# Kernel tuning notes

Hardware: AMD Instinct MI355X
Metric: run time of the kernel (lower is better)

The kernel has to match this reference:

```python
import jax, jax.numpy as jnp
import numpy as np

P = 196608  # number of sample points (N rays x D samples)
N = 2048    # number of rays
K = 8       # number of slot instances
ZD = 64     # network latent dim
N_FREQ = 5
N_FREQ_VIEW = 3
IN_DIM = 33 + 64   # pos-emb (33) + slot feat (64)
VIEW_DIM = 21      # view pos-emb


def sin_emb(x, n_freq):
    # x: (P, 3) -> (P, 3 + 3*2*n_freq); order per freq: sin then cos (matches torch loop)
    freqs = 2.0 ** jnp.arange(n_freq, dtype=x.dtype)          # linspace(0, n_freq-1, n_freq)
    xf = x[:, None, :] * freqs[None, :, None]                  # (P, F, 3)
    e = jnp.stack([jnp.sin(xf), jnp.cos(xf)], axis=2)          # (P, F, 2, 3)
    return jnp.concatenate([x, e.reshape(x.shape[0], -1)], axis=1)


def _lin(x, W, b):
    return x @ W.T + b


def setup_inputs() -> dict:
    key = jax.random.key(0)
    ks = iter(jax.random.split(key, 40))
    def W(o, i):
        return jax.random.normal(next(ks), (o, i), jnp.float32) * (1.0 / np.sqrt(i))
    def b(o):
        return jnp.zeros((o,), jnp.float32)
    inp = {
        "sampling_coor": jax.random.uniform(next(ks), (P, 3), jnp.float32, -1.0, 1.0),
        "sampling_view": jax.random.normal(next(ks), (N, 3), jnp.float32),
        "slots": jax.random.normal(next(ks), (1, K, 64), jnp.float32),
        "raw_density": jax.random.normal(next(ks), (K, P), jnp.float32),
        "act_shift": jnp.zeros((1,), jnp.float32),
        "Wb0": W(ZD, IN_DIM), "bb0": b(ZD),
        "Wb1": W(ZD, ZD), "bb1": b(ZD),
        "Wb2": W(ZD, ZD), "bb2": b(ZD),
        "Wa0": W(ZD, ZD + IN_DIM), "ba0": b(ZD),
        "Wa1": W(ZD, ZD), "ba1": b(ZD),
        "Wa2": W(ZD, ZD), "ba2": b(ZD),
        "Wl": W(ZD, ZD), "bl": b(ZD),                 # after_latent
        "Wv": W(ZD // 2, VIEW_DIM + ZD), "bv": b(ZD // 2),  # views_linears
        "Wc0": W(ZD // 4, ZD // 2), "bc0": b(ZD // 4),      # color[0]
        "Wc1": W(3, ZD // 4), "bc1": b(3),                  # color[2]
        "ray_id": jnp.sort(jax.random.randint(next(ks), (P,), 0, N)).astype(jnp.int64),
    }
    return inp


def reference(sampling_coor, sampling_view, slots, raw_density, act_shift,
              Wb0, bb0, Wb1, bb1, Wb2, bb2,
              Wa0, ba0, Wa1, ba1, Wa2, ba2,
              Wl, bl, Wv, bv, Wc0, bc0, Wc1, bc1,
              ray_id):
    Kk = raw_density.shape[0]
    Pp = sampling_coor.shape[0]
    relu = jax.nn.relu

    coor_emb = sin_emb(sampling_coor, N_FREQ)                    # (P, 33)
    view_emb = sin_emb(sampling_view, N_FREQ_VIEW)[ray_id, :]    # (P, 21) gathered per point

    # broadcast to (K, P, .) instead of flattening to (K*P, .)
    query_ex = jnp.broadcast_to(coor_emb[None], (Kk, Pp, coor_emb.shape[1]))
    slots_ex = jnp.broadcast_to(slots[0][:, None, :], (Kk, Pp, slots.shape[2]))
    inp = jnp.concatenate([query_ex, slots_ex], axis=-1)         # (K, P, 97)

    tmp = relu(_lin(inp, Wb0, bb0))
    tmp = relu(_lin(tmp, Wb1, bb1))
    tmp = relu(_lin(tmp, Wb2, bb2))
    tmp = relu(_lin(jnp.concatenate([inp, tmp], axis=-1), Wa0, ba0))  # skip concat (K,P,161)
    tmp = relu(_lin(tmp, Wa1, ba1))
    tmp = relu(_lin(tmp, Wa2, ba2))
    latent = _lin(tmp, Wl, bl)                                   # (K, P, 64)

    qv = jnp.broadcast_to(view_emb[None], (Kk, Pp, view_emb.shape[1]))
    h = relu(_lin(jnp.concatenate([latent, qv], axis=-1), Wv, bv))
    h = relu(_lin(h, Wc0, bc0))
    raw_rgb_logits = _lin(h, Wc1, bc1)                           # (K, P, 3)

    raw_masks = jax.nn.softplus(raw_density[..., None] + act_shift)  # (K, P, 1)
    raw_sigma = raw_masks                                        # dens_noise = 0.0
    raw_rgb = (jnp.tanh(raw_rgb_logits) + 1.0) / 2.0             # (K, P, 3)

    masks = raw_masks / (raw_masks.sum(axis=0) + 1e-5)           # (K, P, 1)
    raw_rgb_all = (raw_rgb * masks).sum(axis=0)                  # (P, 3)
    raw_sigma_all = (raw_sigma * masks).sum(axis=0)[..., 0]      # (P,)
    return (raw_rgb_all, raw_sigma_all, raw_rgb, raw_sigma[..., 0])
```

## Files before the change

### kernel.cpp

```cpp
#include <hip/hip_runtime.h>
#include <hip/hip_bf16.h>
#include <math.h>

#define PP 196608
#define NK 8

#define O_SIGALL 589824
#define O_RGB    786432
#define O_SIG    5505024

typedef __attribute__((ext_vector_type(8))) short short8;
typedef __attribute__((ext_vector_type(4))) float f32x4;
typedef __attribute__((ext_vector_type(4))) unsigned uint4v;

#define FBB0   0
#define FBA0   512
#define FBB1   1024
#define FBB2   1088
#define FBA1   1152
#define FBA2   1216
#define FBL    1280
#define FBV    1344
#define FBC0   1376
#define FBC1   1392
#define FW32B0 1408
#define FW32A0 1472

#define FB0 0
#define FB1 2048
#define FB2 6144
#define FA0 10240
#define FA1 16384
#define FA2 20480
#define FL  24576
#define FV  28672
#define FC0 31744
#define FC1 32256

#define WS_BYTES 71680

__device__ __forceinline__ short bfr(float f) {
    unsigned u = __builtin_bit_cast(unsigned, f);
    unsigned r = (u + 0x7FFFu + ((u >> 16) & 1u)) >> 16;
    return (short)r;
}

__device__ __forceinline__ unsigned pk2(float a, float b) {
    __hip_bfloat162 h = __float22bfloat162_rn(float2{a, b});
    unsigned r;
    __builtin_memcpy(&r, &h, sizeof(r));
    return r;
}

__device__ __forceinline__ int tau(int p) {
    return 16 * ((p >> 2) & 1) + 4 * (p >> 3) + (p & 3);
}

__device__ __forceinline__ float pe_elem(int j, float c0, float c1, float c2, int jmax) {
    int r = j - 3;
    int rf = r < 0 ? 0 : r;
    int f = rf / 6;
    int t = rf - 6 * f;
    int comp = (j < 3) ? j : (t >= 3 ? t - 3 : t);
    float c = (comp == 0) ? c0 : ((comp == 1) ? c1 : c2);
    float x = c * (float)(1 << f);
    float val = (t < 3) ? sinf(x) : cosf(x);
    if (j < 3) val = c;
    return (j < jmax) ? val : 0.f;
}

__device__ __forceinline__ float softplus_(float d) {
    return fmaxf(d, 0.f) + log1pf(expf(-fabsf(d)));
}

#define MFMA(a, b, c) __builtin_amdgcn_mfma_f32_16x16x32_bf16(a, b, c, 0, 0, 0)

__global__ void prep_kernel(
    const float* __restrict__ slots,
    const float* __restrict__ Wb0, const float* __restrict__ bb0,
    const float* __restrict__ Wb1, const float* __restrict__ bb1,
    const float* __restrict__ Wb2, const float* __restrict__ bb2,
    const float* __restrict__ Wa0, const float* __restrict__ ba0,
    const float* __restrict__ Wa1, const float* __restrict__ ba1,
    const float* __restrict__ Wa2, const float* __restrict__ ba2,
    const float* __restrict__ Wl,  const float* __restrict__ bl,
    const float* __restrict__ Wv,  const float* __restrict__ bv,
    const float* __restrict__ Wc0, const float* __restrict__ bc0,
    const float* __restrict__ Wc1, const float* __restrict__ bc1,
    char* __restrict__ ws)
{
    float* wsF = (float*)ws;
    short* wsS = (short*)(ws + 6144);
    const int tid = threadIdx.x;

    for (int idx = tid; idx < 512; idx += 256) {
        int k = idx >> 6, j = idx & 63;
        const float* sl = slots + k * 64;
        float a = bb0[j];
        const float* w0 = Wb0 + j * 97 + 33;
        for (int i = 0; i < 64; ++i) a = fmaf(w0[i], sl[i], a);
        wsF[FBB0 + idx] = a;
        float b = ba0[j];
        const float* w1 = Wa0 + j * 161 + 33;
        for (int i = 0; i < 64; ++i) b = fmaf(w1[i], sl[i], b);
        wsF[FBA0 + idx] = b;
    }
    for (int idx = tid; idx < 64; idx += 256) {
        wsF[FBB1 + idx] = bb1[idx];
        wsF[FBB2 + idx] = bb2[idx];
        wsF[FBA1 + idx] = ba1[idx];
        wsF[FBA2 + idx] = ba2[idx];
        wsF[FBL  + idx] = bl[idx];
        wsF[FW32B0 + idx] = Wb0[idx * 97 + 32];
        wsF[FW32A0 + idx] = Wa0[idx * 161 + 32];
        if (idx < 32) wsF[FBV + idx] = bv[idx];
        if (idx < 16) { wsF[FBC0 + idx] = bc0[idx];
                        wsF[FBC1 + idx] = (idx < 3) ? bc1[idx] : 0.f; }
    }
    for (int idx = tid; idx < 2048; idx += 256) {
        int frag = idx >> 9, rem = idx & 511, L = rem >> 3, i = rem & 7;
        int r = 16 * frag + (L & 15);
        int cif = 8 * (L >> 4) + i;
        wsS[FB0 + idx] = bfr(Wb0[r * 97 + tau(cif)]);
    }
#define PREP64(FOFF, W) \
    for (int idx = tid; idx < 4096; idx += 256) { \
        int frag = idx >> 9, rem = idx & 511, L = rem >> 3, i = rem & 7; \
        int t = frag >> 1, s = frag & 1; \
        int r = 16 * t + (L & 15); \
        int cif = 8 * (L >> 4) + i; \
        int C = 32 * s + cif; \
        int lc = (C & ~31) + tau(C & 31); \
        wsS[(FOFF) + idx] = bfr(W[r * 64 + lc]); }
    PREP64(FB1, Wb1)
    PREP64(FB2, Wb2)
    PREP64(FA1, Wa1)
    PREP64(FA2, Wa2)
    PREP64(FL,  Wl)
#undef PREP64
    for (int idx = tid; idx < 6144; idx += 256) {
        int frag = idx >> 9, rem = idx & 511, L = rem >> 3, i = rem & 7;
        int t = frag / 3, s = frag % 3;
        int r = 16 * t + (L & 15);
        int cif = 8 * (L >> 4) + i;
        float v;
        if (s == 0) v = Wa0[r * 161 + tau(cif)];
        else {
            int lc = (s == 1 ? 64 : 96) + tau(cif);
            v = Wa0[r * 161 + 33 + lc];
        }
        wsS[FA0 + idx] = bfr(v);
    }
    for (int idx = tid; idx < 3072; idx += 256) {
        int frag = idx >> 9, rem = idx & 511, L = rem >> 3, i = rem & 7;
        int t = frag / 3, s = frag % 3;
        int r = 16 * t + (L & 15);
        int cif = 8 * (L >> 4) + i;
        int C = 32 * s + cif;
        int lc = (C & ~31) + tau(C & 31);
        wsS[FV + idx] = bfr(lc < 85 ? Wv[r * 85 + lc] : 0.f);
    }
    for (int idx = tid; idx < 512; idx += 256) {
        int L = idx >> 3, i = idx & 7;
        int r = L & 15;
        int cif = 8 * (L >> 4) + i;
        int lc = tau(cif);
        wsS[FC0 + idx] = bfr(Wc0[r * 32 + lc]);
        wsS[FC1 + idx] = bfr((r < 3 && lc < 16) ? Wc1[r * 16 + lc] : 0.f);
    }
}

#define FRAG(base, f) (*(const short8*)(shS + (base) + (f) * 512 + l * 8))
#define BIA(off, t)   (*(const f32x4*)(shF + (off) + 16 * (t) + g4))

#define PACKP(cA, cB, dst) { uint4v u_; \
  u_[0] = pk2(fmaxf((cA)[0],0.f), fmaxf((cA)[1],0.f)); \
  u_[1] = pk2(fmaxf((cA)[2],0.f), fmaxf((cA)[3],0.f)); \
  u_[2] = pk2(fmaxf((cB)[0],0.f), fmaxf((cB)[1],0.f)); \
  u_[3] = pk2(fmaxf((cB)[2],0.f), fmaxf((cB)[3],0.f)); \
  dst = __builtin_bit_cast(short8, u_); }

#define PACKN(cA, cB, dst) { uint4v u_; \
  u_[0] = pk2((cA)[0], (cA)[1]); \
  u_[1] = pk2((cA)[2], (cA)[3]); \
  u_[2] = pk2((cB)[0], (cB)[1]); \
  u_[3] = pk2((cB)[2], (cB)[3]); \
  dst = __builtin_bit_cast(short8, u_); }

#define ADD32(c, wv) { (c)[0]=fmaf((wv)[0],cosv,(c)[0]); (c)[1]=fmaf((wv)[1],cosv,(c)[1]); \
                       (c)[2]=fmaf((wv)[2],cosv,(c)[2]); (c)[3]=fmaf((wv)[3],cosv,(c)[3]); }

#define LAYER64_1(FB, BOFF, PK) { \
  short8 A00=FRAG(FB,0), A01=FRAG(FB,1), A10=FRAG(FB,2), A11=FRAG(FB,3); \
  short8 A20=FRAG(FB,4), A21=FRAG(FB,5), A30=FRAG(FB,6), A31=FRAG(FB,7); \
  f32x4 c0=BIA(BOFF,0), c1=BIA(BOFF,1), c2=BIA(BOFF,2), c3=BIA(BOFF,3); \
  c0=MFMA(A00,p0,c0); c1=MFMA(A10,p0,c1); c2=MFMA(A20,p0,c2); c3=MFMA(A30,p0,c3); \
  c0=MFMA(A01,p1,c0); c1=MFMA(A11,p1,c1); c2=MFMA(A21,p1,c2); c3=MFMA(A31,p1,c3); \
  PK(c0,c1,p0); PK(c2,c3,p1); }

__global__ __launch_bounds__(512, 4) void decoder_kernel(
    const float* __restrict__ coor,
    const float* __restrict__ view,
    const float* __restrict__ dens,
    const float* __restrict__ act_shift,
    const int*   __restrict__ ray_id,
    const char*  __restrict__ ws,
    float* __restrict__ out)
{
    __shared__ __align__(16) char sh[WS_BYTES];
    const float* shF = (const float*)sh;
    const short* shS = (const short*)(sh + 6144);

    const int tid = threadIdx.x;
    const int l   = tid & 63;
    const int l15 = l & 15;
    const int g   = (l >> 4) & 3;
    const int g4  = g * 4;
    const int p   = blockIdx.x * 128 + (tid >> 6) * 16 + l15;

    {
        f32x4* dst = (f32x4*)sh;
        const f32x4* src = (const f32x4*)ws;
        for (int i = tid; i < WS_BYTES / 16; i += 512) dst[i] = src[i];
    }

    short8 embB0;
    float cosv;
    {
        float c0 = coor[p * 3 + 0], c1 = coor[p * 3 + 1], c2 = coor[p * 3 + 2];
        #pragma unroll
        for (int i = 0; i < 8; ++i) {
            int j = ((i >> 2) * 16) + 4 * g + (i & 3);
            embB0[i] = bfr(pe_elem(j, c0, c1, c2, 33));
        }
        cosv = cosf(c2 * 16.f);
    }
    short8 vembB;
    {
        int rid = ray_id[p];
        float v0 = view[rid * 3 + 0], v1 = view[rid * 3 + 1], v2 = view[rid * 3 + 2];
        #pragma unroll
        for (int i = 0; i < 8; ++i) {
            int j = ((i >> 2) * 16) + 4 * g + (i & 3);
            vembB[i] = bfr(pe_elem(j, v0, v1, v2, 21));
        }
    }
    float shift = act_shift[0];

    __syncthreads();

    #pragma unroll 1
    for (int k = 0; k < NK; ++k) {
        asm volatile("" ::: "memory");

        {
            float d_ = dens[k * PP + p] + shift;
            float sp = softplus_(d_);
            if (l < 16) out[O_SIG + k * PP + p] = sp;
        }

        short8 p0, p1;

        {
            short8 A0 = FRAG(FB0, 0), A1 = FRAG(FB0, 1), A2 = FRAG(FB0, 2), A3 = FRAG(FB0, 3);
            f32x4 wv0 = BIA(FW32B0, 0), wv1 = BIA(FW32B0, 1), wv2 = BIA(FW32B0, 2), wv3 = BIA(FW32B0, 3);
            f32x4 c0 = *(const f32x4*)(shF + FBB0 + k * 64 +  0 + g4);
            f32x4 c1 = *(const f32x4*)(shF + FBB0 + k * 64 + 16 + g4);
            f32x4 c2 = *(const f32x4*)(shF + FBB0 + k * 64 + 32 + g4);
            f32x4 c3 = *(const f32x4*)(shF + FBB0 + k * 64 + 48 + g4);
            c0 = MFMA(A0, embB0, c0); c1 = MFMA(A1, embB0, c1);
            c2 = MFMA(A2, embB0, c2); c3 = MFMA(A3, embB0, c3);
            ADD32(c0, wv0) ADD32(c1, wv1) ADD32(c2, wv2) ADD32(c3, wv3)
            PACKP(c0, c1, p0); PACKP(c2, c3, p1);
        }
        LAYER64_1(FB1, FBB1, PACKP)
        LAYER64_1(FB2, FBB2, PACKP)
        {
            short8 E0 = FRAG(FA0, 0), K00 = FRAG(FA0, 1),  K01 = FRAG(FA0, 2);
            short8 E1 = FRAG(FA0, 3), K10 = FRAG(FA0, 4),  K11 = FRAG(FA0, 5);
            short8 E2 = FRAG(FA0, 6), K20 = FRAG(FA0, 7),  K21 = FRAG(FA0, 8);
            short8 E3 = FRAG(FA0, 9), K30 = FRAG(FA0, 10), K31 = FRAG(FA0, 11);
            f32x4 wv0 = BIA(FW32A0, 0), wv1 = BIA(FW32A0, 1), wv2 = BIA(FW32A0, 2), wv3 = BIA(FW32A0, 3);
            f32x4 c0 = *(const f32x4*)(shF + FBA0 + k * 64 +  0 + g4);
            f32x4 c1 = *(const f32x4*)(shF + FBA0 + k * 64 + 16 + g4);
            f32x4 c2 = *(const f32x4*)(shF + FBA0 + k * 64 + 32 + g4);
            f32x4 c3 = *(const f32x4*)(shF + FBA0 + k * 64 + 48 + g4);
            c0 = MFMA(E0, embB0, c0); c1 = MFMA(E1, embB0, c1);
            c2 = MFMA(E2, embB0, c2); c3 = MFMA(E3, embB0, c3);
            c0 = MFMA(K00, p0, c0); c1 = MFMA(K10, p0, c1);
            c2 = MFMA(K20, p0, c2); c3 = MFMA(K30, p0, c3);
            c0 = MFMA(K01, p1, c0); c1 = MFMA(K11, p1, c1);
            c2 = MFMA(K21, p1, c2); c3 = MFMA(K31, p1, c3);
            ADD32(c0, wv0) ADD32(c1, wv1) ADD32(c2, wv2) ADD32(c3, wv3)
            PACKP(c0, c1, p0); PACKP(c2, c3, p1);
        }
        LAYER64_1(FA1, FBA1, PACKP)
        LAYER64_1(FA2, FBA2, PACKP)
        LAYER64_1(FL,  FBL,  PACKN)
        {
            f32x4 cv0 = BIA(FBV, 0), cv1 = BIA(FBV, 1);
            cv0 = MFMA(FRAG(FV, 0), p0, cv0);  cv1 = MFMA(FRAG(FV, 3), p0, cv1);
            cv0 = MFMA(FRAG(FV, 1), p1, cv0);  cv1 = MFMA(FRAG(FV, 4), p1, cv1);
            cv0 = MFMA(FRAG(FV, 2), vembB, cv0); cv1 = MFMA(FRAG(FV, 5), vembB, cv1);
            short8 vB;
            PACKP(cv0, cv1, vB);
            f32x4 cc = BIA(FBC0, 0);
            cc = MFMA(FRAG(FC0, 0), vB, cc);
            short8 cB;
            { uint4v u_;
              u_[0] = pk2(fmaxf(cc[0],0.f), fmaxf(cc[1],0.f));
              u_[1] = pk2(fmaxf(cc[2],0.f), fmaxf(cc[3],0.f));
              u_[2] = 0u; u_[3] = 0u;
              cB = __builtin_bit_cast(short8, u_); }
            f32x4 cf = BIA(FBC1, 0);
            cf = MFMA(FRAG(FC1, 0), cB, cf);
            if (l < 16) {
                int base = O_RGB + (k * PP + p) * 3;
                out[base + 0] = (tanhf(cf[0]) + 1.f) * 0.5f;
                out[base + 1] = (tanhf(cf[1]) + 1.f) * 0.5f;
                out[base + 2] = (tanhf(cf[2]) + 1.f) * 0.5f;
            }
        }
    }
}

__global__ __launch_bounds__(256) void reduce_kernel(float* __restrict__ out)
{
    const int p = blockIdx.x * 256 + threadIdx.x;
    float s0 = out[O_SIG + 0 * PP + p];
    float s1 = out[O_SIG + 1 * PP + p];
    float s2 = out[O_SIG + 2 * PP + p];
    float s3 = out[O_SIG + 3 * PP + p];
    float s4 = out[O_SIG + 4 * PP + p];
    float s5 = out[O_SIG + 5 * PP + p];
    float s6 = out[O_SIG + 6 * PP + p];
    float s7 = out[O_SIG + 7 * PP + p];
    float msum = s0 + s1 + s2 + s3 + s4 + s5 + s6 + s7;
    float inv = 1.f / (msum + 1e-5f);
    float mk2 = s0*s0 + s1*s1 + s2*s2 + s3*s3 + s4*s4 + s5*s5 + s6*s6 + s7*s7;
    out[O_SIGALL + p] = mk2 * inv;
    float a0 = 0.f, a1 = 0.f, a2 = 0.f;
#define RK(i, sv) { float wk = (sv) * inv; \
    int b_ = O_RGB + ((i) * PP + p) * 3; \
    a0 = fmaf(wk, out[b_ + 0], a0); \
    a1 = fmaf(wk, out[b_ + 1], a1); \
    a2 = fmaf(wk, out[b_ + 2], a2); }
    RK(0, s0) RK(1, s1) RK(2, s2) RK(3, s3)
    RK(4, s4) RK(5, s5) RK(6, s6) RK(7, s7)
#undef RK
    out[p * 3 + 0] = a0;
    out[p * 3 + 1] = a1;
    out[p * 3 + 2] = a2;
}

extern "C" void kernel_launch(void* const* d_in, const int* in_sizes, int n_in,
                              void* d_out, int out_size, void* d_ws, size_t ws_size,
                              hipStream_t stream) {
    const float* coor  = (const float*)d_in[0];
    const float* view  = (const float*)d_in[1];
    const float* slots = (const float*)d_in[2];
    const float* dens  = (const float*)d_in[3];
    const float* shf   = (const float*)d_in[4];
    const float* Wb0 = (const float*)d_in[5];  const float* bb0 = (const float*)d_in[6];
    const float* Wb1 = (const float*)d_in[7];  const float* bb1 = (const float*)d_in[8];
    const float* Wb2 = (const float*)d_in[9];  const float* bb2 = (const float*)d_in[10];
    const float* Wa0 = (const float*)d_in[11]; const float* ba0 = (const float*)d_in[12];
    const float* Wa1 = (const float*)d_in[13]; const float* ba1 = (const float*)d_in[14];
    const float* Wa2 = (const float*)d_in[15]; const float* ba2 = (const float*)d_in[16];
    const float* Wl  = (const float*)d_in[17]; const float* bl  = (const float*)d_in[18];
    const float* Wv  = (const float*)d_in[19]; const float* bv  = (const float*)d_in[20];
    const float* Wc0 = (const float*)d_in[21]; const float* bc0 = (const float*)d_in[22];
    const float* Wc1 = (const float*)d_in[23]; const float* bc1 = (const float*)d_in[24];
    const int*   ray = (const int*)d_in[25];
    float* out = (float*)d_out;

    prep_kernel<<<dim3(1), dim3(256), 0, stream>>>(
        slots, Wb0, bb0, Wb1, bb1, Wb2, bb2,
        Wa0, ba0, Wa1, ba1, Wa2, ba2,
        Wl, bl, Wv, bv, Wc0, bc0, Wc1, bc1, (char*)d_ws);

    decoder_kernel<<<dim3(PP / 128), dim3(512), 0, stream>>>(
        coor, view, dens, shf, ray, (const char*)d_ws, out);

    reduce_kernel<<<dim3(PP / 256), dim3(256), 0, stream>>>(out);
}
```

Measured before the change: 201.6 us.

## Process two slots per loop iteration to share weight fragment loads

```diff
diff --git a/kernel.cpp b/kernel.cpp
--- a/kernel.cpp
+++ b/kernel.cpp
@@ -172,6 +172,7 @@
 
 #define FRAG(base, f) (*(const short8*)(shS + (base) + (f) * 512 + l * 8))
 #define BIA(off, t)   (*(const f32x4*)(shF + (off) + 16 * (t) + g4))
+#define BSLOT(off, kidx, t) (*(const f32x4*)(shF + (off) + (kidx) * 64 + 16 * (t) + g4))
 
 #define PACKP(cA, cB, dst) { uint4v u_; \
   u_[0] = pk2(fmaxf((cA)[0],0.f), fmaxf((cA)[1],0.f)); \
@@ -190,13 +191,40 @@
 #define ADD32(c, wv) { (c)[0]=fmaf((wv)[0],cosv,(c)[0]); (c)[1]=fmaf((wv)[1],cosv,(c)[1]); \
                        (c)[2]=fmaf((wv)[2],cosv,(c)[2]); (c)[3]=fmaf((wv)[3],cosv,(c)[3]); }
 
-#define LAYER64_1(FB, BOFF, PK) { \
+#define LAYER64_2(FB, BOFF, PK) { \
   short8 A00=FRAG(FB,0), A01=FRAG(FB,1), A10=FRAG(FB,2), A11=FRAG(FB,3); \
   short8 A20=FRAG(FB,4), A21=FRAG(FB,5), A30=FRAG(FB,6), A31=FRAG(FB,7); \
-  f32x4 c0=BIA(BOFF,0), c1=BIA(BOFF,1), c2=BIA(BOFF,2), c3=BIA(BOFF,3); \
-  c0=MFMA(A00,p0,c0); c1=MFMA(A10,p0,c1); c2=MFMA(A20,p0,c2); c3=MFMA(A30,p0,c3); \
-  c0=MFMA(A01,p1,c0); c1=MFMA(A11,p1,c1); c2=MFMA(A21,p1,c2); c3=MFMA(A31,p1,c3); \
-  PK(c0,c1,p0); PK(c2,c3,p1); }
+  f32x4 b0_=BIA(BOFF,0), b1_=BIA(BOFF,1), b2_=BIA(BOFF,2), b3_=BIA(BOFF,3); \
+  f32x4 c0=b0_, c1=b1_, c2=b2_, c3=b3_; \
+  c0=MFMA(A00,p0a,c0); c1=MFMA(A10,p0a,c1); c2=MFMA(A20,p0a,c2); c3=MFMA(A30,p0a,c3); \
+  c0=MFMA(A01,p1a,c0); c1=MFMA(A11,p1a,c1); c2=MFMA(A21,p1a,c2); c3=MFMA(A31,p1a,c3); \
+  PK(c0,c1,p0a); PK(c2,c3,p1a); \
+  f32x4 d0=b0_, d1=b1_, d2=b2_, d3=b3_; \
+  d0=MFMA(A00,p0b,d0); d1=MFMA(A10,p0b,d1); d2=MFMA(A20,p0b,d2); d3=MFMA(A30,p0b,d3); \
+  d0=MFMA(A01,p1b,d0); d1=MFMA(A11,p1b,d1); d2=MFMA(A21,p1b,d2); d3=MFMA(A31,p1b,d3); \
+  PK(d0,d1,p0b); PK(d2,d3,p1b); }
+
+#define TAIL1(PA, PB, KIDX) { \
+  f32x4 cv0 = BIA(FBV, 0), cv1 = BIA(FBV, 1); \
+  cv0 = MFMA(AV00, PA, cv0); cv1 = MFMA(AV10, PA, cv1); \
+  cv0 = MFMA(AV01, PB, cv0); cv1 = MFMA(AV11, PB, cv1); \
+  cv0 = MFMA(AV02, vembB, cv0); cv1 = MFMA(AV12, vembB, cv1); \
+  short8 vB; PACKP(cv0, cv1, vB); \
+  f32x4 cc = BIA(FBC0, 0); \
+  cc = MFMA(AC0f, vB, cc); \
+  short8 cB; \
+  { uint4v u_; \
+    u_[0] = pk2(fmaxf(cc[0],0.f), fmaxf(cc[1],0.f)); \
+    u_[1] = pk2(fmaxf(cc[2],0.f), fmaxf(cc[3],0.f)); \
+    u_[2] = 0u; u_[3] = 0u; \
+    cB = __builtin_bit_cast(short8, u_); } \
+  f32x4 cf = BIA(FBC1, 0); \
+  cf = MFMA(AC1f, cB, cf); \
+  if (l < 16) { \
+      int base_ = O_RGB + ((KIDX) * PP + p) * 3; \
+      out[base_ + 0] = (tanhf(cf[0]) + 1.f) * 0.5f; \
+      out[base_ + 1] = (tanhf(cf[1]) + 1.f) * 0.5f; \
+      out[base_ + 2] = (tanhf(cf[2]) + 1.f) * 0.5f; } }
 
 __global__ __launch_bounds__(512, 4) void decoder_kernel(
     const float* __restrict__ coor,
@@ -250,76 +278,73 @@
     __syncthreads();
 
     #pragma unroll 1
-    for (int k = 0; k < NK; ++k) {
+    for (int kk = 0; kk < 4; ++kk) {
         asm volatile("" ::: "memory");
 
+        const int k0 = 2 * kk, k1 = 2 * kk + 1;
+
         {
-            float d_ = dens[k * PP + p] + shift;
-            float sp = softplus_(d_);
-            if (l < 16) out[O_SIG + k * PP + p] = sp;
-        }
-
-        short8 p0, p1;
+            float da = dens[k0 * PP + p] + shift;
+            float sa = softplus_(da);
+            if (l < 16) out[O_SIG + k0 * PP + p] = sa;
+            float db = dens[k1 * PP + p] + shift;
+            float sb = softplus_(db);
+            if (l < 16) out[O_SIG + k1 * PP + p] = sb;
+        }
+
+        short8 p0a, p1a, p0b, p1b;
 
         {
             short8 A0 = FRAG(FB0, 0), A1 = FRAG(FB0, 1), A2 = FRAG(FB0, 2), A3 = FRAG(FB0, 3);
             f32x4 wv0 = BIA(FW32B0, 0), wv1 = BIA(FW32B0, 1), wv2 = BIA(FW32B0, 2), wv3 = BIA(FW32B0, 3);
-            f32x4 c0 = *(const f32x4*)(shF + FBB0 + k * 64 +  0 + g4);
-            f32x4 c1 = *(const f32x4*)(shF + FBB0 + k * 64 + 16 + g4);
-            f32x4 c2 = *(const f32x4*)(shF + FBB0 + k * 64 + 32 + g4);
-            f32x4 c3 = *(const f32x4*)(shF + FBB0 + k * 64 + 48 + g4);
-            c0 = MFMA(A0, embB0, c0); c1 = MFMA(A1, embB0, c1);
-            c2 = MFMA(A2, embB0, c2); c3 = MFMA(A3, embB0, c3);
-            ADD32(c0, wv0) ADD32(c1, wv1) ADD32(c2, wv2) ADD32(c3, wv3)
-            PACKP(c0, c1, p0); PACKP(c2, c3, p1);
-        }
-        LAYER64_1(FB1, FBB1, PACKP)
-        LAYER64_1(FB2, FBB2, PACKP)
+            f32x4 z = {0.f, 0.f, 0.f, 0.f};
+            f32x4 t0 = MFMA(A0, embB0, z), t1 = MFMA(A1, embB0, z);
+            f32x4 t2 = MFMA(A2, embB0, z), t3 = MFMA(A3, embB0, z);
+            ADD32(t0, wv0) ADD32(t1, wv1) ADD32(t2, wv2) ADD32(t3, wv3)
+            f32x4 c0 = t0 + BSLOT(FBB0, k0, 0), c1 = t1 + BSLOT(FBB0, k0, 1);
+            f32x4 c2 = t2 + BSLOT(FBB0, k0, 2), c3 = t3 + BSLOT(FBB0, k0, 3);
+            PACKP(c0, c1, p0a); PACKP(c2, c3, p1a);
+            f32x4 d0 = t0 + BSLOT(FBB0, k1, 0), d1 = t1 + BSLOT(FBB0, k1, 1);
+            f32x4 d2 = t2 + BSLOT(FBB0, k1, 2), d3 = t3 + BSLOT(FBB0, k1, 3);
+            PACKP(d0, d1, p0b); PACKP(d2, d3, p1b);
+        }
+        LAYER64_2(FB1, FBB1, PACKP)
+        LAYER64_2(FB2, FBB2, PACKP)
         {
             short8 E0 = FRAG(FA0, 0), K00 = FRAG(FA0, 1),  K01 = FRAG(FA0, 2);
             short8 E1 = FRAG(FA0, 3), K10 = FRAG(FA0, 4),  K11 = FRAG(FA0, 5);
             short8 E2 = FRAG(FA0, 6), K20 = FRAG(FA0, 7),  K21 = FRAG(FA0, 8);
             short8 E3 = FRAG(FA0, 9), K30 = FRAG(FA0, 10), K31 = FRAG(FA0, 11);
             f32x4 wv0 = BIA(FW32A0, 0), wv1 = BIA(FW32A0, 1), wv2 = BIA(FW32A0, 2), wv3 = BIA(FW32A0, 3);
-            f32x4 c0 = *(const f32x4*)(shF + FBA0 + k * 64 +  0 + g4);
-            f32x4 c1 = *(const f32x4*)(shF + FBA0 + k * 64 + 16 + g4);
-            f32x4 c2 = *(const f32x4*)(shF + FBA0 + k * 64 + 32 + g4);
-            f32x4 c3 = *(const f32x4*)(shF + FBA0 + k * 64 + 48 + g4);
-            c0 = MFMA(E0, embB0, c0); c1 = MFMA(E1, embB0, c1);
-            c2 = MFMA(E2, embB0, c2); c3 = MFMA(E3, embB0, c3);
-            c0 = MFMA(K00, p0, c0); c1 = MFMA(K10, p0, c1);
-            c2 = MFMA(K20, p0, c2); c3 = MFMA(K30, p0, c3);
-            c0 = MFMA(K01, p1, c0); c1 = MFMA(K11, p1, c1);
-            c2 = MFMA(K21, p1, c2); c3 = MFMA(K31, p1, c3);
-            ADD32(c0, wv0) ADD32(c1, wv1) ADD32(c2, wv2) ADD32(c3, wv3)
-            PACKP(c0, c1, p0); PACKP(c2, c3, p1);
-        }
-        LAYER64_1(FA1, FBA1, PACKP)
-        LAYER64_1(FA2, FBA2, PACKP)
-        LAYER64_1(FL,  FBL,  PACKN)
+            f32x4 z = {0.f, 0.f, 0.f, 0.f};
+            f32x4 s0 = MFMA(E0, embB0, z), s1 = MFMA(E1, embB0, z);
+            f32x4 s2 = MFMA(E2, embB0, z), s3 = MFMA(E3, embB0, z);
+            ADD32(s0, wv0) ADD32(s1, wv1) ADD32(s2, wv2) ADD32(s3, wv3)
+            f32x4 c0 = s0 + BSLOT(FBA0, k0, 0), c1 = s1 + BSLOT(FBA0, k0, 1);
+            f32x4 c2 = s2 + BSLOT(FBA0, k0, 2), c3 = s3 + BSLOT(FBA0, k0, 3);
+            c0 = MFMA(K00, p0a, c0); c1 = MFMA(K10, p0a, c1);
+            c2 = MFMA(K20, p0a, c2); c3 = MFMA(K30, p0a, c3);
+            c0 = MFMA(K01, p1a, c0); c1 = MFMA(K11, p1a, c1);
+            c2 = MFMA(K21, p1a, c2); c3 = MFMA(K31, p1a, c3);
+            PACKP(c0, c1, p0a); PACKP(c2, c3, p1a);
+            f32x4 d0 = s0 + BSLOT(FBA0, k1, 0), d1 = s1 + BSLOT(FBA0, k1, 1);
+            f32x4 d2 = s2 + BSLOT(FBA0, k1, 2), d3 = s3 + BSLOT(FBA0, k1, 3);
+            d0 = MFMA(K00, p0b, d0); d1 = MFMA(K10, p0b, d1);
+            d2 = MFMA(K20, p0b, d2); d3 = MFMA(K30, p0b, d3);
+            d0 = MFMA(K01, p1b, d0); d1 = MFMA(K11, p1b, d1);
+            d2 = MFMA(K21, p1b, d2); d3 = MFMA(K31, p1b, d3);
+            PACKP(d0, d1, p0b); PACKP(d2, d3, p1b);
+        }
+        LAYER64_2(FA1, FBA1, PACKP)
+        LAYER64_2(FA2, FBA2, PACKP)
+        LAYER64_2(FL,  FBL,  PACKN)
         {
-            f32x4 cv0 = BIA(FBV, 0), cv1 = BIA(FBV, 1);
-            cv0 = MFMA(FRAG(FV, 0), p0, cv0);  cv1 = MFMA(FRAG(FV, 3), p0, cv1);
-            cv0 = MFMA(FRAG(FV, 1), p1, cv0);  cv1 = MFMA(FRAG(FV, 4), p1, cv1);
-            cv0 = MFMA(FRAG(FV, 2), vembB, cv0); cv1 = MFMA(FRAG(FV, 5), vembB, cv1);
-            short8 vB;
-            PACKP(cv0, cv1, vB);
-            f32x4 cc = BIA(FBC0, 0);
-            cc = MFMA(FRAG(FC0, 0), vB, cc);
-            short8 cB;
-            { uint4v u_;
-              u_[0] = pk2(fmaxf(cc[0],0.f), fmaxf(cc[1],0.f));
-              u_[1] = pk2(fmaxf(cc[2],0.f), fmaxf(cc[3],0.f));
-              u_[2] = 0u; u_[3] = 0u;
-              cB = __builtin_bit_cast(short8, u_); }
-            f32x4 cf = BIA(FBC1, 0);
-            cf = MFMA(FRAG(FC1, 0), cB, cf);
-            if (l < 16) {
-                int base = O_RGB + (k * PP + p) * 3;
-                out[base + 0] = (tanhf(cf[0]) + 1.f) * 0.5f;
-                out[base + 1] = (tanhf(cf[1]) + 1.f) * 0.5f;
-                out[base + 2] = (tanhf(cf[2]) + 1.f) * 0.5f;
-            }
+            short8 AV00 = FRAG(FV, 0), AV10 = FRAG(FV, 3);
+            short8 AV01 = FRAG(FV, 1), AV11 = FRAG(FV, 4);
+            short8 AV02 = FRAG(FV, 2), AV12 = FRAG(FV, 5);
+            short8 AC0f = FRAG(FC0, 0), AC1f = FRAG(FC1, 0);
+            TAIL1(p0a, p1a, k0)
+            TAIL1(p0b, p1b, k1)
         }
     }
 }
```

After: 197.0 us. 1.02x faster.
